# Optimization experiments

Measured on AMD Instinct MI355X. Metric: run time of the kernel, lower is better.

Reference implementation:

```python
import jax, jax.numpy as jnp
import numpy as np

N = 100000   # nodes
E = 1600000  # edges
DIN = 100    # input feature dim
D = 64       # hidden dim per GCN layer
G = 512      # graphs in batch
EPS = 1e-5


def setup_inputs() -> dict:
    key = jax.random.key(0)
    ks = jax.random.split(key, 16)
    inp = {}
    inp["x"] = jax.random.normal(ks[0], (N, DIN), dtype=jnp.float32)
    inp["edge_index"] = jax.random.randint(ks[1], (2, E), 0, N)
    inp["edge_weight"] = jax.random.uniform(ks[2], (E,), dtype=jnp.float32)
    inp["batch"] = jnp.sort(jax.random.randint(ks[3], (N,), 0, G))
    dims = [DIN, D, D, D]
    for i in range(3):
        fan_in = dims[i]
        inp[f"w{i}"] = jax.random.normal(ks[4 + i], (dims[i], dims[i + 1]), dtype=jnp.float32) / np.sqrt(fan_in)
        inp[f"b{i}"] = jnp.zeros((dims[i + 1],), dtype=jnp.float32)
        inp[f"g{i}"] = jnp.ones((dims[i + 1],), dtype=jnp.float32)   # BN scale
        inp[f"be{i}"] = jnp.zeros((dims[i + 1],), dtype=jnp.float32)  # BN shift
    inp["out_w"] = jax.random.normal(ks[7], (D, 1), dtype=jnp.float32) / np.sqrt(D)
    inp["out_b"] = jnp.zeros((1,), dtype=jnp.float32)
    return inp


def reference(x, edge_index, edge_weight, batch,
              w0, b0, g0, be0, w1, b1, g1, be1, w2, b2, g2, be2,
              out_w, out_b):
    src, dst = edge_index[0], edge_index[1]
    n = x.shape[0]
    # GCN symmetric normalization with self-loops (PyG gcn_norm, fill_value=1)
    deg = jnp.zeros((n,), dtype=x.dtype).at[dst].add(edge_weight) + 1.0
    dinv = jax.lax.rsqrt(deg)
    norm = edge_weight * dinv[src] * dinv[dst]   # [E]
    self_coeff = dinv * dinv                      # 1/deg, self-loop norm  [N]

    def gcn_bn_relu(h, w, b, g, be):
        h = h @ w + b                                             # linear transform [N,D]
        msg = norm[:, None] * h[src]                              # gather + weight [E,D]
        agg = jnp.zeros_like(h).at[dst].add(msg) + h * self_coeff[:, None]
        mean = agg.mean(axis=0)
        var = agg.var(axis=0)                                     # biased var (torch BN)
        hn = (agg - mean) * jax.lax.rsqrt(var + EPS) * g + be
        return jax.nn.relu(hn)                                    # dropout p=0 -> identity

    h = gcn_bn_relu(x, w0, b0, g0, be0)
    h = gcn_bn_relu(h, w1, b1, g1, be1)
    h = gcn_bn_relu(h, w2, b2, g2, be2)

    # global mean pool per graph
    sums = jax.ops.segment_sum(h, batch, num_segments=G)
    counts = jax.ops.segment_sum(jnp.ones((n, 1), dtype=h.dtype), batch, num_segments=G)
    pooled = sums / jnp.maximum(counts, 1.0)
    return pooled @ out_w + out_b
```

## Files before the change

### kernel.cpp

```cpp
#include <hip/hip_runtime.h>
#include <hip/hip_fp16.h>
#include <cstdint>

#define DH 64
#define EPSV 1e-5f
#define GBLK 2048
#define NBUK 256
#define BROWS 512
#define BINJ 8
#define CAP 12288

typedef _Float16 half8 __attribute__((ext_vector_type(8)));
typedef float f32x4 __attribute__((ext_vector_type(4)));

__global__ void k_gcur0(unsigned* __restrict__ gcur0) {
  gcur0[threadIdx.x] = (unsigned)(threadIdx.x * CAP);
}

__global__ __launch_bounds__(256) void k_xhalf(const float* __restrict__ x,
                                               unsigned short* __restrict__ xh,
                                               int N_, int K) {
  const int cpr = K / 4;
  size_t i = blockIdx.x * 256ull + threadIdx.x;
  if (i >= (size_t)N_ * cpr) return;
  int row = (int)(i / cpr), c0 = (int)(i % cpr) * 4;
  float4 v = *(const float4*)&x[(size_t)row * K + c0];
  ushort4 h;
  h.x = __half_as_ushort(__float2half(v.x));
  h.y = __half_as_ushort(__float2half(v.y));
  h.z = __half_as_ushort(__float2half(v.z));
  h.w = __half_as_ushort(__float2half(v.w));
  *(ushort4*)&xh[(size_t)row * 128 + c0] = h;
  if (c0 == K - 4) {
    ushort4 z4 = {0, 0, 0, 0};
    uint4 z16 = {0, 0, 0, 0};
    *(ushort4*)&xh[(size_t)row * 128 + K] = z4;
    *(uint4*)&xh[(size_t)row * 128 + K + 4] = z16;
    *(uint4*)&xh[(size_t)row * 128 + K + 12] = z16;
    *(uint4*)&xh[(size_t)row * 128 + K + 20] = z16;
  }
}

__global__ void k_wt(const float* __restrict__ W, unsigned short* __restrict__ wt,
                     int Kreal, int KP) {
  int idx = blockIdx.x * 256 + threadIdx.x;
  if (idx >= 64 * KP) return;
  int c = idx / KP, k = idx % KP;
  float v = (k < Kreal) ? W[k * DH + c] : 0.f;
  wt[idx] = __half_as_ushort(__float2half(v));
}

__global__ __launch_bounds__(256) void k_bin0(
    const int* __restrict__ src, const int* __restrict__ dst,
    const float* __restrict__ ew, unsigned* __restrict__ gcur0,
    unsigned long long* __restrict__ bstage, int E_) {
  __shared__ unsigned cntL[NBUK], offL[NBUK], runL[NBUK];
  const int t = threadIdx.x;
  const int base = blockIdx.x * (256 * BINJ);
  cntL[t] = 0;
  runL[t] = 0;
  __syncthreads();
  unsigned hi[BINJ], lo[BINJ];
  int bb[BINJ];
#pragma unroll
  for (int j = 0; j < BINJ; ++j) {
    int e = base + j * 256 + t;
    bb[j] = -1;
    if (e < E_) {
      int q = dst[e];
      hi[j] = ((unsigned)(q & (BROWS - 1)) << 17) | (unsigned)src[e];
      lo[j] = __float_as_uint(ew[e]);
      bb[j] = q >> 9;
      atomicAdd(&cntL[bb[j]], 1u);
    }
  }
  __syncthreads();
  offL[t] = cntL[t] ? atomicAdd(&gcur0[t], cntL[t]) : 0u;
  __syncthreads();
#pragma unroll
  for (int j = 0; j < BINJ; ++j) {
    if (bb[j] >= 0) {
      unsigned p = offL[bb[j]] + atomicAdd(&runL[bb[j]], 1u);
      bstage[p] = ((unsigned long long)hi[j] << 32) | lo[j];
    }
  }
}

__global__ __launch_bounds__(256) void k_bcnt(
    const unsigned long long* __restrict__ bstage, const unsigned* __restrict__ gcur0,
    int* __restrict__ cnt, float* __restrict__ dinv, float* __restrict__ sc, int N_) {
  __shared__ unsigned cntL[BROWS], degL[BROWS];
  const int b = blockIdx.x, t = threadIdx.x;
  for (int i = t; i < BROWS; i += 256) {
    cntL[i] = 0;
    degL[i] = 0;
  }
  __syncthreads();
  const unsigned beg = (unsigned)(b * CAP), end = gcur0[b];
  for (unsigned p = beg + t; p < end; p += 256) {
    unsigned long long v = bstage[p];
    unsigned r = (unsigned)(v >> 49);
    float w = __uint_as_float((unsigned)v);
    atomicAdd(&cntL[r], 1u);
    atomicAdd(&degL[r], (unsigned)(w * 16777216.0f));
  }
  __syncthreads();
  for (int i = t; i < BROWS; i += 256) {
    int r = b * BROWS + i;
    if (r < N_) {
      float deg = 1.0f + (float)degL[i] * (1.0f / 16777216.0f);
      cnt[r] = (int)cntL[i];
      dinv[r] = rsqrtf(deg);
      sc[r] = 1.0f / deg;
    }
  }
}

__global__ __launch_bounds__(256) void k_scan1(const int* __restrict__ cnt,
                                               int* __restrict__ out,
                                               int* __restrict__ bsums,
                                               int N_, int n1) {
  __shared__ int sm[256];
  const int t = threadIdx.x;
  const int base = blockIdx.x * 1024 + t * 4;
  int v[4], lsum = 0;
#pragma unroll
  for (int j = 0; j < 4; ++j) {
    int i = base + j;
    v[j] = (i < N_) ? cnt[i] : 0;
    lsum += v[j];
  }
  sm[t] = lsum;
  __syncthreads();
  for (int o = 1; o < 256; o <<= 1) {
    int x = (t >= o) ? sm[t - o] : 0;
    __syncthreads();
    if (t >= o) sm[t] += x;
    __syncthreads();
  }
  int run = sm[t] - lsum;
#pragma unroll
  for (int j = 0; j < 4; ++j) {
    int i = base + j;
    if (i < n1) out[i] = run;
    run += v[j];
  }
  if (t == 255) bsums[blockIdx.x] = sm[255];
}

__global__ __launch_bounds__(256) void k_scan2(int* __restrict__ bsums, int nb) {
  __shared__ int sm[256];
  int t = threadIdx.x;
  int v = (t < nb) ? bsums[t] : 0;
  sm[t] = v;
  __syncthreads();
  for (int o = 1; o < 256; o <<= 1) {
    int x = (t >= o) ? sm[t - o] : 0;
    __syncthreads();
    if (t >= o) sm[t] += x;
    __syncthreads();
  }
  if (t < nb) bsums[t] = sm[t] - v;
}

__global__ void k_scan3(int* __restrict__ out, const int* __restrict__ bsums, int n1) {
  int i = blockIdx.x * blockDim.x + threadIdx.x;
  if (i < n1) out[i] += bsums[i >> 10];
}

__global__ __launch_bounds__(256) void k_fin(
    const unsigned long long* __restrict__ bstage, const int* __restrict__ rowstart,
    const unsigned* __restrict__ gcur0, const float* __restrict__ dinv,
    unsigned* __restrict__ elist, int N_) {
  __shared__ unsigned lcur[BROWS];
  __shared__ int rsL[BROWS];
  __shared__ float dvL[BROWS];
  const int b = blockIdx.x, t = threadIdx.x;
  const int r0 = b * BROWS;
  for (int i = t; i < BROWS; i += 256) {
    lcur[i] = 0;
    int r = r0 + i;
    dvL[i] = (r < N_) ? dinv[r] : 0.f;
    rsL[i] = (r < N_) ? rowstart[r] : 0;
  }
  __syncthreads();
  const unsigned beg = (unsigned)(b * CAP), end = gcur0[b];
  for (unsigned p = beg + t; p < end; p += 256) {
    unsigned long long v = bstage[p];
    unsigned hi = (unsigned)(v >> 32);
    unsigned r = hi >> 17;
    unsigned s = hi & 0x1FFFFu;
    float w = __uint_as_float((unsigned)v);
    float nm = w * dinv[s] * dvL[r];
    unsigned h15 = (unsigned)__half_as_ushort(__float2half(nm));
    unsigned slot = (unsigned)rsL[r] + atomicAdd(&lcur[r], 1u);
    elist[slot] = (h15 << 17) | s;
  }
}

__global__ void k_gbound(const int* __restrict__ batch, int* __restrict__ gstart,
                         int N_, int G_) {
  int i = blockIdx.x * blockDim.x + threadIdx.x;
  if (i >= N_) return;
  int b = batch[i];
  if (i == 0) {
    for (int g = 0; g <= b; ++g) gstart[g] = 0;
  }
  int nb = (i + 1 < N_) ? batch[i + 1] : G_;
  for (int g = b + 1; g <= nb; ++g) gstart[g] = i + 1;
}

template <int KP, int FUSE>
__global__ __launch_bounds__(256) void k_gemm_mfma(
    const unsigned short* __restrict__ Aa, const unsigned short* __restrict__ wt,
    const float* __restrict__ bias, const float* __restrict__ stats,
    const float* __restrict__ gam, const float* __restrict__ bet,
    unsigned short* __restrict__ Hu, int n, float invN) {
  __shared__ unsigned short Ah[128 * KP];
  __shared__ unsigned short Bt[64 * KP];
  __shared__ float saL[DH], sbL[DH];
  const int tid = threadIdx.x;
  const int r0 = blockIdx.x * 128;
  if (FUSE) {
    if (tid < DH) {
      float mean = stats[tid] * invN;
      float var = stats[DH + tid] * invN - mean * mean;
      float a = rsqrtf(var + EPSV) * gam[tid];
      saL[tid] = a;
      sbL[tid] = bet[tid] - mean * a;
    }
    __syncthreads();
  }
  constexpr int KC = KP / 8;
  for (int ci = tid; ci < 128 * KC; ci += 256) {
    int row = ci / KC, kc = ci % KC, k0 = kc * 8;
    int gr = r0 + row;
    uint4 av = {0, 0, 0, 0};
    if (gr < n) av = *(const uint4*)&Aa[(size_t)gr * KP + k0];
    if (FUSE) {
      const unsigned short* ap = (const unsigned short*)&av;
      unsigned short ov[8];
#pragma unroll
      for (int j = 0; j < 8; ++j) {
        int k = k0 + j;
        float a = __half2float(__ushort_as_half(ap[j]));
        ov[j] = __half_as_ushort(__float2half(fmaxf(a * saL[k] + sbL[k], 0.f)));
      }
      av = *(uint4*)ov;
    }
    *(uint4*)&Ah[row * KP + (k0 ^ ((row & 7) * 8))] = av;
  }
  for (int ci = tid; ci < 64 * KC; ci += 256) {
    int c = ci / KC, kc = ci % KC, k0 = kc * 8;
    uint4 wv = *(const uint4*)&wt[c * KP + k0];
    *(uint4*)&Bt[c * KP + (k0 ^ ((c & 7) * 8))] = wv;
  }
  __syncthreads();
  const int w = tid >> 6, l = tid & 63;
  const int lr = l & 15, lg = l >> 4;
  f32x4 acc[2][4];
#pragma unroll
  for (int a1 = 0; a1 < 2; ++a1)
#pragma unroll
    for (int a2 = 0; a2 < 4; ++a2) acc[a1][a2] = (f32x4){0.f, 0.f, 0.f, 0.f};
#pragma unroll
  for (int ks = 0; ks < KP / 32; ++ks) {
    const int k0 = ks * 32 + lg * 8;
    half8 av[2], bv[4];
#pragma unroll
    for (int rf = 0; rf < 2; ++rf) {
      int row = w * 32 + rf * 16 + lr;
      av[rf] = *(const half8*)&Ah[row * KP + (k0 ^ ((row & 7) * 8))];
    }
#pragma unroll
    for (int cf = 0; cf < 4; ++cf) {
      int col = cf * 16 + lr;
      bv[cf] = *(const half8*)&Bt[col * KP + (k0 ^ ((col & 7) * 8))];
    }
#pragma unroll
    for (int rf = 0; rf < 2; ++rf)
#pragma unroll
      for (int cf = 0; cf < 4; ++cf)
        acc[rf][cf] =
            __builtin_amdgcn_mfma_f32_16x16x32_f16(av[rf], bv[cf], acc[rf][cf], 0, 0, 0);
  }
#pragma unroll
  for (int rf = 0; rf < 2; ++rf) {
#pragma unroll
    for (int cf = 0; cf < 4; ++cf) {
      int col = cf * 16 + lr;
      float bcol = bias[col];
#pragma unroll
      for (int i = 0; i < 4; ++i) {
        int row = r0 + w * 32 + rf * 16 + lg * 4 + i;
        if (row < n)
          Hu[(size_t)row * DH + col] = __half_as_ushort(__float2half(acc[rf][cf][i] + bcol));
      }
    }
  }
}

__global__ __launch_bounds__(256) void k_gather(
    const unsigned* __restrict__ elist, const int* __restrict__ rowstart,
    const unsigned short* __restrict__ Hu, const float* __restrict__ sc,
    unsigned short* __restrict__ AGGu, float* __restrict__ statp, int n) {
  const int wid = threadIdx.x >> 6;
  const int d = threadIdx.x & 63;
  const int gw = blockIdx.x * 4 + wid;
  const int nw = gridDim.x * 4;
  float s = 0.f, ss = 0.f;
  for (int row = gw; row < n; row += nw) {
    const int rs = rowstart[row], re = rowstart[row + 1];
    float acc = __half2float(__ushort_as_half(Hu[(size_t)row * DH + d])) * sc[row];
    for (int base = rs; base < re; base += 64) {
      const int rem = re - base;
      unsigned eL = 0u;
      if (d < rem) eL = __builtin_nontemporal_load(&elist[base + d]);
      const int m = rem < 64 ? ((rem + 7) & ~7) : 64;
      for (int j = 0; j < m; j += 8) {
        unsigned e[8];
        float v[8];
#pragma unroll
        for (int jj = 0; jj < 8; ++jj) e[jj] = __shfl(eL, j + jj, 64);
#pragma unroll
        for (int jj = 0; jj < 8; ++jj)
          v[jj] = __half2float(__ushort_as_half(Hu[(size_t)(e[jj] & 0x1FFFFu) * DH + d]));
#pragma unroll
        for (int jj = 0; jj < 8; ++jj) {
          float nm = __half2float(__ushort_as_half((unsigned short)(e[jj] >> 17)));
          acc = fmaf(nm, v[jj], acc);
        }
      }
    }
    __builtin_nontemporal_store(__half_as_ushort(__float2half(acc)),
                                &AGGu[(size_t)row * DH + d]);
    s += acc;
    ss += acc * acc;
  }
  __shared__ float sm[4][DH], sm2[4][DH];
  sm[wid][d] = s;
  sm2[wid][d] = ss;
  __syncthreads();
  if (threadIdx.x < DH) {
    float a = sm[0][d] + sm[1][d] + sm[2][d] + sm[3][d];
    float b = sm2[0][d] + sm2[1][d] + sm2[2][d] + sm2[3][d];
    __builtin_nontemporal_store(a, &statp[(size_t)blockIdx.x * 128 + d]);
    __builtin_nontemporal_store(b, &statp[(size_t)blockIdx.x * 128 + DH + d]);
  }
}

__global__ __launch_bounds__(256) void k_redstats(const float* __restrict__ statp,
                                                  float* __restrict__ stats, int nblk) {
  const int t = blockIdx.x;
  float s = 0.f;
  for (int b = threadIdx.x; b < nblk; b += 256) s += statp[(size_t)b * 128 + t];
#pragma unroll
  for (int o = 32; o > 0; o >>= 1) s += __shfl_down(s, o, 64);
  __shared__ float sm[4];
  if ((threadIdx.x & 63) == 0) sm[threadIdx.x >> 6] = s;
  __syncthreads();
  if (threadIdx.x == 0) stats[t] = sm[0] + sm[1] + sm[2] + sm[3];
}

__global__ __launch_bounds__(256) void k_poolhead(
    const unsigned short* __restrict__ AGGu, const float* __restrict__ stats,
    const float* __restrict__ gam, const float* __restrict__ bet,
    const float* __restrict__ ow, const int* __restrict__ gstart,
    const float* __restrict__ ob, float* __restrict__ out, float invN) {
  const int g = blockIdx.x;
  const int gs = gstart[g], ge = gstart[g + 1];
  const int wid = threadIdx.x >> 6;
  const int d = threadIdx.x & 63;
  float mean = stats[d] * invN;
  float var = stats[DH + d] * invN - mean * mean;
  float sa = rsqrtf(var + EPSV) * gam[d];
  float sb = bet[d] - mean * sa;
  const float w = ow[d];
  float acc = 0.f;
  for (int row = gs + wid; row < ge; row += 4) {
    float v = __half2float(__ushort_as_half(AGGu[(size_t)row * DH + d]));
    acc += fmaxf(v * sa + sb, 0.f) * w;
  }
#pragma unroll
  for (int off = 32; off > 0; off >>= 1) acc += __shfl_down(acc, off, 64);
  __shared__ float sm[4];
  if (d == 0) sm[wid] = acc;
  __syncthreads();
  if (threadIdx.x == 0) {
    float s = sm[0] + sm[1] + sm[2] + sm[3];
    float cnt = (float)(ge - gs);
    out[g] = s / fmaxf(cnt, 1.0f) + ob[0];
  }
}

extern "C" void kernel_launch(void* const* d_in, const int* in_sizes, int n_in,
                              void* d_out, int out_size, void* d_ws, size_t ws_size,
                              hipStream_t stream) {
  const float* x    = (const float*)d_in[0];
  const int*   ei   = (const int*)d_in[1];
  const float* ew   = (const float*)d_in[2];
  const int*   batch= (const int*)d_in[3];
  const float* w0   = (const float*)d_in[4];
  const float* b0   = (const float*)d_in[5];
  const float* g0   = (const float*)d_in[6];
  const float* be0  = (const float*)d_in[7];
  const float* w1   = (const float*)d_in[8];
  const float* b1   = (const float*)d_in[9];
  const float* g1   = (const float*)d_in[10];
  const float* be1  = (const float*)d_in[11];
  const float* w2   = (const float*)d_in[12];
  const float* b2   = (const float*)d_in[13];
  const float* g2   = (const float*)d_in[14];
  const float* be2  = (const float*)d_in[15];
  const float* ow   = (const float*)d_in[16];
  const float* ob   = (const float*)d_in[17];

  const int N_  = in_sizes[3];
  const int E_  = in_sizes[2];
  const int DIN_= in_sizes[0] / N_;
  const int G_  = out_size;
  const int* srcIdx = ei;
  const int* dstIdx = ei + E_;
  const int n1 = N_ + 1;

  float* ws = (float*)d_ws;
  size_t off = 0;
  unsigned long long* bstage = (unsigned long long*)(ws + off);
  off += (size_t)2 * NBUK * CAP;
  unsigned* elist = (unsigned*)(ws + off); off += E_;
  float* dinv     = ws + off; off += N_;
  float* sc       = ws + off; off += N_;
  int*   cnt      = (int*)(ws + off); off += N_;
  int*   rowstart = (int*)(ws + off); off += n1 + 1;
  int*   bsums    = (int*)(ws + off); off += 256;
  unsigned* gcur0 = (unsigned*)(ws + off); off += NBUK;
  int*   gstart   = (int*)(ws + off); off += G_ + 1;
  unsigned short* hbuf = (unsigned short*)(ws + off); off += (size_t)N_ * 32;
  unsigned short* aggb = (unsigned short*)(ws + off); off += (size_t)N_ * 32;
  unsigned short* xh = (unsigned short*)(ws + off); off += (size_t)N_ * 64;
  unsigned short* wt0 = (unsigned short*)(ws + off); off += 64 * 128 / 2;
  unsigned short* wt1 = (unsigned short*)(ws + off); off += 64 * 64 / 2;
  unsigned short* wt2 = (unsigned short*)(ws + off); off += 64 * 64 / 2;
  float* stats    = ws + off; off += 2 * DH;
  float* statp    = ws + off; off += (size_t)GBLK * 128;
  (void)ws_size; (void)n_in;

  k_xhalf<<<(int)(((size_t)N_ * (DIN_ / 4) + 255) / 256), 256, 0, stream>>>(x, xh, N_, DIN_);
  k_wt<<<(64 * 128 + 255) / 256, 256, 0, stream>>>(w0, wt0, DIN_, 128);
  k_wt<<<(64 * 64 + 255) / 256, 256, 0, stream>>>(w1, wt1, DH, 64);
  k_wt<<<(64 * 64 + 255) / 256, 256, 0, stream>>>(w2, wt2, DH, 64);

  k_gcur0<<<1, NBUK, 0, stream>>>(gcur0);
  k_bin0<<<(E_ + 256 * BINJ - 1) / (256 * BINJ), 256, 0, stream>>>(
      srcIdx, dstIdx, ew, gcur0, bstage, E_);
  k_bcnt<<<NBUK, 256, 0, stream>>>(bstage, gcur0, cnt, dinv, sc, N_);

  const int nb = (n1 + 1023) / 1024;
  k_scan1<<<nb, 256, 0, stream>>>(cnt, rowstart, bsums, N_, n1);
  k_scan2<<<1, 256, 0, stream>>>(bsums, nb);
  k_scan3<<<(n1 + 255) / 256, 256, 0, stream>>>(rowstart, bsums, n1);

  k_fin<<<NBUK, 256, 0, stream>>>(bstage, rowstart, gcur0, dinv, elist, N_);

  k_gbound<<<(N_ + 255) / 256, 256, 0, stream>>>(batch, gstart, N_, G_);

  const float* Bl[3]  = {b0, b1, b2};
  const float* Gl[3]  = {g0, g1, g2};
  const float* BeL[3] = {be0, be1, be2};
  const unsigned short* Wt[3] = {wt0, wt1, wt2};

  const float invN = 1.0f / (float)N_;
  const int gblk = (N_ + 127) / 128;

  for (int l = 0; l < 3; ++l) {
    if (l == 0) {
      k_gemm_mfma<128, 0><<<gblk, 256, 0, stream>>>(
          xh, Wt[0], Bl[0], stats, nullptr, nullptr, hbuf, N_, invN);
    } else {
      k_gemm_mfma<64, 1><<<gblk, 256, 0, stream>>>(
          aggb, Wt[l], Bl[l], stats, Gl[l - 1], BeL[l - 1], hbuf, N_, invN);
    }
    k_gather<<<GBLK, 256, 0, stream>>>(elist, rowstart, hbuf, sc, aggb, statp, N_);
    k_redstats<<<128, 256, 0, stream>>>(statp, stats, GBLK);
  }

  k_poolhead<<<G_, 256, 0, stream>>>(aggb, stats, g2, be2, ow, gstart, ob,
                                     (float*)d_out, invN);
}
```

Before: 336.8 us.

## Fuse fp32-to-half input conversion into first GEMM and merge setup kernels

The first-layer GEMM now reads the fp32 input features directly and converts them to half while staging into shared memory, which removes the separate conversion kernel and its padded half-precision buffer round trip. The weight transposes, the bucket cursor init and the graph-boundary computation are merged into one setup kernel to cut launch count. The fp32 loads are float4 pairs aligned on the 100-wide rows, and the partial tail chunk falls back to scalar loads.

```diff
diff --git a/kernel.cpp b/kernel.cpp
--- a/kernel.cpp
+++ b/kernel.cpp
@@ -13,41 +13,40 @@
 typedef _Float16 half8 __attribute__((ext_vector_type(8)));
 typedef float f32x4 __attribute__((ext_vector_type(4)));
 
-__global__ void k_gcur0(unsigned* __restrict__ gcur0) {
-  gcur0[threadIdx.x] = (unsigned)(threadIdx.x * CAP);
-}
-
-__global__ __launch_bounds__(256) void k_xhalf(const float* __restrict__ x,
-                                               unsigned short* __restrict__ xh,
-                                               int N_, int K) {
-  const int cpr = K / 4;
-  size_t i = blockIdx.x * 256ull + threadIdx.x;
-  if (i >= (size_t)N_ * cpr) return;
-  int row = (int)(i / cpr), c0 = (int)(i % cpr) * 4;
-  float4 v = *(const float4*)&x[(size_t)row * K + c0];
-  ushort4 h;
-  h.x = __half_as_ushort(__float2half(v.x));
-  h.y = __half_as_ushort(__float2half(v.y));
-  h.z = __half_as_ushort(__float2half(v.z));
-  h.w = __half_as_ushort(__float2half(v.w));
-  *(ushort4*)&xh[(size_t)row * 128 + c0] = h;
-  if (c0 == K - 4) {
-    ushort4 z4 = {0, 0, 0, 0};
-    uint4 z16 = {0, 0, 0, 0};
-    *(ushort4*)&xh[(size_t)row * 128 + K] = z4;
-    *(uint4*)&xh[(size_t)row * 128 + K + 4] = z16;
-    *(uint4*)&xh[(size_t)row * 128 + K + 12] = z16;
-    *(uint4*)&xh[(size_t)row * 128 + K + 20] = z16;
-  }
-}
-
-__global__ void k_wt(const float* __restrict__ W, unsigned short* __restrict__ wt,
-                     int Kreal, int KP) {
-  int idx = blockIdx.x * 256 + threadIdx.x;
-  if (idx >= 64 * KP) return;
-  int c = idx / KP, k = idx % KP;
-  float v = (k < Kreal) ? W[k * DH + c] : 0.f;
-  wt[idx] = __half_as_ushort(__float2half(v));
+__global__ __launch_bounds__(256) void k_setup(
+    const int* __restrict__ batch, int* __restrict__ gstart,
+    unsigned* __restrict__ gcur0,
+    const float* __restrict__ w0, const float* __restrict__ w1,
+    const float* __restrict__ w2, unsigned short* __restrict__ wt0,
+    unsigned short* __restrict__ wt1, unsigned short* __restrict__ wt2,
+    int N_, int G_, int DIN_, int nbN) {
+  const int b = blockIdx.x, t = threadIdx.x;
+  if (b < nbN) {
+    int i = b * 256 + t;
+    if (i >= N_) return;
+    int bb = batch[i];
+    if (i == 0) {
+      for (int g = 0; g <= bb; ++g) gstart[g] = 0;
+    }
+    int nb2 = (i + 1 < N_) ? batch[i + 1] : G_;
+    for (int g = bb + 1; g <= nb2; ++g) gstart[g] = i + 1;
+  } else if (b == nbN) {
+    if (t < NBUK) gcur0[t] = (unsigned)(t * CAP);
+  } else {
+    int idx = (b - nbN - 1) * 256 + t;
+    if (idx < 64 * 128) {
+      int c = idx / 128, k = idx % 128;
+      wt0[idx] = __half_as_ushort(__float2half(k < DIN_ ? w0[k * DH + c] : 0.f));
+    } else if (idx < 64 * 128 + 64 * 64) {
+      int l2 = idx - 64 * 128;
+      int c = l2 / 64, k = l2 % 64;
+      wt1[l2] = __half_as_ushort(__float2half(w1[k * DH + c]));
+    } else if (idx < 64 * 128 + 2 * 64 * 64) {
+      int l2 = idx - 64 * 128 - 64 * 64;
+      int c = l2 / 64, k = l2 % 64;
+      wt2[l2] = __half_as_ushort(__float2half(w2[k * DH + c]));
+    }
+  }
 }
 
 __global__ __launch_bounds__(256) void k_bin0(
@@ -198,24 +197,12 @@
   }
 }
 
-__global__ void k_gbound(const int* __restrict__ batch, int* __restrict__ gstart,
-                         int N_, int G_) {
-  int i = blockIdx.x * blockDim.x + threadIdx.x;
-  if (i >= N_) return;
-  int b = batch[i];
-  if (i == 0) {
-    for (int g = 0; g <= b; ++g) gstart[g] = 0;
-  }
-  int nb = (i + 1 < N_) ? batch[i + 1] : G_;
-  for (int g = b + 1; g <= nb; ++g) gstart[g] = i + 1;
-}
-
 template <int KP, int FUSE>
 __global__ __launch_bounds__(256) void k_gemm_mfma(
-    const unsigned short* __restrict__ Aa, const unsigned short* __restrict__ wt,
+    const void* __restrict__ Ap, const unsigned short* __restrict__ wt,
     const float* __restrict__ bias, const float* __restrict__ stats,
     const float* __restrict__ gam, const float* __restrict__ bet,
-    unsigned short* __restrict__ Hu, int n, float invN) {
+    unsigned short* __restrict__ Hu, int n, int Kreal, float invN) {
   __shared__ unsigned short Ah[128 * KP];
   __shared__ unsigned short Bt[64 * KP];
   __shared__ float saL[DH], sbL[DH];
@@ -236,8 +223,9 @@
     int row = ci / KC, kc = ci % KC, k0 = kc * 8;
     int gr = r0 + row;
     uint4 av = {0, 0, 0, 0};
-    if (gr < n) av = *(const uint4*)&Aa[(size_t)gr * KP + k0];
     if (FUSE) {
+      const unsigned short* Aa = (const unsigned short*)Ap;
+      if (gr < n) av = *(const uint4*)&Aa[(size_t)gr * KP + k0];
       const unsigned short* ap = (const unsigned short*)&av;
       unsigned short ov[8];
 #pragma unroll
@@ -245,6 +233,31 @@
         int k = k0 + j;
         float a = __half2float(__ushort_as_half(ap[j]));
         ov[j] = __half_as_ushort(__float2half(fmaxf(a * saL[k] + sbL[k], 0.f)));
+      }
+      av = *(uint4*)ov;
+    } else {
+      const float* Ax = (const float*)Ap;
+      unsigned short ov[8] = {0, 0, 0, 0, 0, 0, 0, 0};
+      if (gr < n) {
+        if (k0 + 8 <= Kreal) {
+          float4 a = *(const float4*)&Ax[(size_t)gr * Kreal + k0];
+          float4 b = *(const float4*)&Ax[(size_t)gr * Kreal + k0 + 4];
+          ov[0] = __half_as_ushort(__float2half(a.x));
+          ov[1] = __half_as_ushort(__float2half(a.y));
+          ov[2] = __half_as_ushort(__float2half(a.z));
+          ov[3] = __half_as_ushort(__float2half(a.w));
+          ov[4] = __half_as_ushort(__float2half(b.x));
+          ov[5] = __half_as_ushort(__float2half(b.y));
+          ov[6] = __half_as_ushort(__float2half(b.z));
+          ov[7] = __half_as_ushort(__float2half(b.w));
+        } else if (k0 < Kreal) {
+#pragma unroll
+          for (int j = 0; j < 8; ++j) {
+            int k = k0 + j;
+            if (k < Kreal)
+              ov[j] = __half_as_ushort(__float2half(Ax[(size_t)gr * Kreal + k]));
+          }
+        }
       }
       av = *(uint4*)ov;
     }
@@ -437,7 +450,6 @@
   int*   gstart   = (int*)(ws + off); off += G_ + 1;
   unsigned short* hbuf = (unsigned short*)(ws + off); off += (size_t)N_ * 32;
   unsigned short* aggb = (unsigned short*)(ws + off); off += (size_t)N_ * 32;
-  unsigned short* xh = (unsigned short*)(ws + off); off += (size_t)N_ * 64;
   unsigned short* wt0 = (unsigned short*)(ws + off); off += 64 * 128 / 2;
   unsigned short* wt1 = (unsigned short*)(ws + off); off += 64 * 64 / 2;
   unsigned short* wt2 = (unsigned short*)(ws + off); off += 64 * 64 / 2;
@@ -445,12 +457,11 @@
   float* statp    = ws + off; off += (size_t)GBLK * 128;
   (void)ws_size; (void)n_in;
 
-  k_xhalf<<<(int)(((size_t)N_ * (DIN_ / 4) + 255) / 256), 256, 0, stream>>>(x, xh, N_, DIN_);
-  k_wt<<<(64 * 128 + 255) / 256, 256, 0, stream>>>(w0, wt0, DIN_, 128);
-  k_wt<<<(64 * 64 + 255) / 256, 256, 0, stream>>>(w1, wt1, DH, 64);
-  k_wt<<<(64 * 64 + 255) / 256, 256, 0, stream>>>(w2, wt2, DH, 64);
-
-  k_gcur0<<<1, NBUK, 0, stream>>>(gcur0);
+  const int nbN = (N_ + 255) / 256;
+  const int wtBlocks = (64 * 128 + 2 * 64 * 64 + 255) / 256;
+  k_setup<<<nbN + 1 + wtBlocks, 256, 0, stream>>>(
+      batch, gstart, gcur0, w0, w1, w2, wt0, wt1, wt2, N_, G_, DIN_, nbN);
+
   k_bin0<<<(E_ + 256 * BINJ - 1) / (256 * BINJ), 256, 0, stream>>>(
       srcIdx, dstIdx, ew, gcur0, bstage, E_);
   k_bcnt<<<NBUK, 256, 0, stream>>>(bstage, gcur0, cnt, dinv, sc, N_);
@@ -462,8 +473,6 @@
 
   k_fin<<<NBUK, 256, 0, stream>>>(bstage, rowstart, gcur0, dinv, elist, N_);
 
-  k_gbound<<<(N_ + 255) / 256, 256, 0, stream>>>(batch, gstart, N_, G_);
-
   const float* Bl[3]  = {b0, b1, b2};
   const float* Gl[3]  = {g0, g1, g2};
   const float* BeL[3] = {be0, be1, be2};
@@ -475,10 +484,10 @@
   for (int l = 0; l < 3; ++l) {
     if (l == 0) {
       k_gemm_mfma<128, 0><<<gblk, 256, 0, stream>>>(
-          xh, Wt[0], Bl[0], stats, nullptr, nullptr, hbuf, N_, invN);
+          (const void*)x, Wt[0], Bl[0], stats, nullptr, nullptr, hbuf, N_, DIN_, invN);
     } else {
       k_gemm_mfma<64, 1><<<gblk, 256, 0, stream>>>(
-          aggb, Wt[l], Bl[l], stats, Gl[l - 1], BeL[l - 1], hbuf, N_, invN);
+          (const void*)aggb, Wt[l], Bl[l], stats, Gl[l - 1], BeL[l - 1], hbuf, N_, DH, invN);
     }
     k_gather<<<GBLK, 256, 0, stream>>>(elist, rowstart, hbuf, sc, aggb, statp, N_);
     k_redstats<<<128, 256, 0, stream>>>(statp, stats, GBLK);
```

Measured after the change: 326.5 us (median of 2 runs). -3.1%, faster.
